# Kernel optimization log

Hardware: AMD Instinct MI355X
Metric: run time of the kernel (lower is better)

Reference implementation:

```python
import jax, jax.numpy as jnp
import numpy as np

B, C = 262144, 14  # batch, num_labels (CheXpert 14 labels)
MAX_T = C - 1      # max_num_trials
L_PARAM = 14       # self.l
KAPPA = 2.0
RAMP_CAP = 1.8     # 1 - s with s = -0.8


def setup_inputs() -> dict:
    key = jax.random.key(0)
    k1, k2, k3, k4 = jax.random.split(key, 4)
    inp = jax.random.normal(k1, (B, C), dtype=jnp.float32)
    target = jax.random.randint(k2, (B, C), 0, 2, dtype=jnp.int32)
    S = jax.random.uniform(k3, (B,), dtype=jnp.float32)
    # pre-drawn uniforms driving the sequential negative-sampling trials
    rand_u = jax.random.uniform(k4, (B, C, MAX_T), dtype=jnp.float32)
    return {"inp": inp, "target": target, "S": S, "rand_u": rand_u}


def reference(inp, target, S, rand_u):
    # L[i] = sum_{r=1..i+1} 1/r  (harmonic weights), indices 0..L_PARAM-1
    L = jnp.cumsum(1.0 / (jnp.arange(L_PARAM, dtype=inp.dtype) + 1.0))

    neg_mask = target == 0                      # [B,C]
    pos_mask = target == 1                      # [B,C]
    num_neg = neg_mask.sum(axis=1)              # [B]

    # negative label positions packed to the front of each row (stable)
    order = jnp.argsort(jnp.where(neg_mask, 0, 1), axis=1, stable=True)  # [B,C]

    rows = jnp.arange(B)[:, None, None]
    # uniform choice among the num_neg negatives, per (i, j, trial)
    t_idx = jnp.clip((rand_u * num_neg[:, None, None].astype(rand_u.dtype)).astype(jnp.int32),
                     0, jnp.maximum(num_neg - 1, 0)[:, None, None])       # [B,C,T]
    neg_sample = order[rows, t_idx]                                       # [B,C,T]

    # sequential trial loop: stop at first margin >= 0, cap at MAX_T trials
    margins = 1.0 - inp[:, :, None] + inp[rows, neg_sample]               # [B,C,T]
    nonneg = margins >= 0
    first = jnp.argmax(nonneg, axis=2)                                    # 0 if none
    num_trials = jnp.where(nonneg.any(axis=2), first + 1, MAX_T)          # [B,C]
    r_j = MAX_T // num_trials                                             # floor
    weight = L[r_j]                                                       # [B,C]

    # ramp(1 - inp[i,j] + inp[i,k]) = clip(inp[i,j] - inp[i,k], 0, 1.8)
    pairwise = jnp.clip(inp[:, :, None] - inp[:, None, :], 0.0, RAMP_CAP)  # [B,C(j),C(k)]
    neg_sum = jnp.sum(pairwise * neg_mask[:, None, :].astype(inp.dtype), axis=2)  # [B,C]

    # s_i = 1 for i <= l, else S[i - l]
    idx = jnp.arange(B)
    s_i = jnp.where(idx <= L_PARAM, 1.0, S[jnp.maximum(idx - L_PARAM, 0)])  # [B]

    valid = pos_mask & (num_neg > 0)[:, None]  # skip positives with no negatives
    loss_warp = jnp.sum(s_i[:, None] * jnp.where(valid, weight * neg_sum, 0.0))

    # kappa term: ramp(target * inp) over all labels
    ramp_k = jnp.clip(1.0 - target.astype(inp.dtype) * inp, 0.0, RAMP_CAP)
    loss_kappa = KAPPA * jnp.sum(s_i[:, None] * ramp_k)

    return loss_warp + loss_kappa
```

## Files before the change

### kernel.cpp

```cpp
#include <hip/hip_runtime.h>

#define CC   14
#define MAXT 13
#define TPB  256
#define RAMP_CAP 1.8f

__global__ __launch_bounds__(TPB) void rwl_kernel(
    const float* __restrict__ inp, const int* __restrict__ target,
    const float* __restrict__ S, const float* __restrict__ rand_u,
    float* __restrict__ out, int B)
{
    __shared__ float s_red[4];
    const int tid = threadIdx.x;
    const int row = blockIdx.x * TPB + tid;

    constexpr float H2  = 1.0f + 0.5f;
    constexpr float H3  = H2  + (1.0f/3.0f);
    constexpr float H4  = H3  + 0.25f;
    constexpr float H5  = H4  + 0.2f;
    constexpr float H6  = H5  + (1.0f/6.0f);
    constexpr float H7  = H6  + (1.0f/7.0f);
    constexpr float H8  = H7  + 0.125f;
    constexpr float H9  = H8  + (1.0f/9.0f);
    constexpr float H10 = H9  + 0.1f;
    constexpr float H11 = H10 + (1.0f/11.0f);
    constexpr float H12 = H11 + (1.0f/12.0f);
    constexpr float H13 = H12 + (1.0f/13.0f);
    constexpr float H14 = H13 + (1.0f/14.0f);

    float total = 0.f;
    if (row < B) {
        const float* xrow = inp + (size_t)row * CC;
        const int*   trow = target + (size_t)row * CC;

        float x[CC];
        #pragma unroll
        for (int k = 0; k < CC; ++k) x[k] = xrow[k];

        unsigned pm = 0; float kap = 0.f;
        #pragma unroll
        for (int k = 0; k < CC; ++k) {
            if (trow[k] != 0) {
                pm |= (1u << k);
                kap += fminf(fmaxf(1.0f - x[k], 0.f), RAMP_CAP);
            } else {
                kap += 1.0f;
            }
        }
        const int nn = CC - __popc(pm);

        float lw = 0.f;
        if (pm != 0u && nn > 0) {
            const float fnn = (float)nn;
            const float* pu = rand_u + (size_t)row * (CC * MAXT);
            #pragma unroll
            for (int j = 0; j < CC; ++j) {
                if ((pm >> j) & 1u) {
                    const float* uj = pu + j * MAXT;
                    float uv[8];
                    #pragma unroll
                    for (int t = 0; t < 8; ++t) uv[t] = uj[t];

                    const float m1 = 1.0f - x[j];
                    float nsum = 0.f; unsigned gm = 0; int cnt = 0;
                    #pragma unroll
                    for (int k = 0; k < CC; ++k) {
                        if (!((pm >> k) & 1u)) {
                            nsum += fminf(fmaxf(x[j] - x[k], 0.f), RAMP_CAP);
                            if (m1 + x[k] >= 0.f) gm |= (1u << cnt);
                            ++cnt;
                        }
                    }

                    unsigned bits = 0;
                    #pragma unroll
                    for (int t = 0; t < 8; ++t) {
                        int ti = (int)(uv[t] * fnn);
                        ti = ti < 0 ? 0 : ti;
                        ti = ti > nn - 1 ? nn - 1 : ti;
                        bits |= ((gm >> ti) & 1u) << t;
                    }
                    if (bits == 0u) {
                        #pragma unroll
                        for (int t = 8; t < MAXT; ++t) {
                            int ti = (int)(uj[t] * fnn);
                            ti = ti < 0 ? 0 : ti;
                            ti = ti > nn - 1 ? nn - 1 : ti;
                            bits |= ((gm >> ti) & 1u) << t;
                        }
                    }
                    const int nt = bits ? __ffs(bits) : MAXT;
                    const float wt = (nt == 1) ? H14 : (nt == 2) ? H7
                                   : (nt == 3) ? H5  : (nt == 4) ? H4
                                   : (nt <= 6) ? H3  : H2;
                    lw += wt * nsum;
                }
            }
        }
        const float si = (row <= 14) ? 1.0f : S[row - 14];
        total = si * (lw + 2.0f * kap);
    }

    #pragma unroll
    for (int off = 32; off > 0; off >>= 1)
        total += __shfl_down(total, off, 64);
    const int wave = tid >> 6;
    if ((tid & 63) == 0) s_red[wave] = total;
    __syncthreads();
    if (tid == 0)
        atomicAdd(out, s_red[0] + s_red[1] + s_red[2] + s_red[3]);
}

extern "C" void kernel_launch(void* const* d_in, const int* in_sizes, int n_in,
                              void* d_out, int out_size, void* d_ws, size_t ws_size,
                              hipStream_t stream) {
    const float* inp    = (const float*)d_in[0];
    const int*   target = (const int*)d_in[1];
    const float* S      = (const float*)d_in[2];
    const float* ru     = (const float*)d_in[3];
    float*       out    = (float*)d_out;
    const int B = in_sizes[2];

    hipMemsetAsync(out, 0, sizeof(float), stream);

    const int blocks = (B + TPB - 1) / TPB;
    rwl_kernel<<<blocks, TPB, 0, stream>>>(inp, target, S, ru, out, B);
}
```

Measured before the change: 55.56 us.

## Process two rows per thread with alignment-aware vectorized float4 loads

Each thread now handles a pair of rows, with templates on row parity so the 14-wide rows can be read using aligned float4/float2 loads of inputs and targets. The per-label random-uniform reads become three aligned float4 loads, using a compile-time shift that accounts for each label's offset within the 182-float row. The aim is fewer, wider memory transactions and more independent work per thread. In exchange it halves the thread count, roughly doubles register pressure, and over-fetches some unused uniforms.

```diff
diff --git a/kernel.cpp b/kernel.cpp
--- a/kernel.cpp
+++ b/kernel.cpp
@@ -5,101 +5,165 @@
 #define TPB  256
 #define RAMP_CAP 1.8f
 
+constexpr float H2  = 1.0f + 0.5f;
+constexpr float H3  = H2  + (1.0f/3.0f);
+constexpr float H4  = H3  + 0.25f;
+constexpr float H5  = H4  + 0.2f;
+constexpr float H6  = H5  + (1.0f/6.0f);
+constexpr float H7  = H6  + (1.0f/7.0f);
+constexpr float H14 = H7 + 0.125f + (1.0f/9.0f) + 0.1f + (1.0f/11.0f)
+                         + (1.0f/12.0f) + (1.0f/13.0f) + (1.0f/14.0f);
+
+template<int PAR, int J>
+__device__ __forceinline__ void do_label(unsigned pm, int nn, float fnn,
+                                         const float* __restrict__ rowF,
+                                         const float (&x)[CC], float& lw)
+{
+    if ((pm >> J) & 1u) {
+        constexpr int SH = (J + 2 * PAR) & 3;
+        const float* qp = rowF + (13 * J - SH);
+        float4 q0 = *(const float4*)(qp);
+        float4 q1 = *(const float4*)(qp + 4);
+        float4 q2 = *(const float4*)(qp + 8);
+        const float e[12] = {q0.x,q0.y,q0.z,q0.w, q1.x,q1.y,q1.z,q1.w,
+                             q2.x,q2.y,q2.z,q2.w};
+
+        const float m1 = 1.0f - x[J];
+        float nsum = 0.f; unsigned gm = 0; int cnt = 0;
+        #pragma unroll
+        for (int k = 0; k < CC; ++k) {
+            if (!((pm >> k) & 1u)) {
+                nsum += fminf(fmaxf(x[J] - x[k], 0.f), RAMP_CAP);
+                if (m1 + x[k] >= 0.f) gm |= (1u << cnt);
+                ++cnt;
+            }
+        }
+
+        unsigned bits = 0;
+        #pragma unroll
+        for (int t = 0; t < 8; ++t) {
+            int ti = (int)(e[SH + t] * fnn);
+            ti = ti < 0 ? 0 : ti;
+            ti = ti > nn - 1 ? nn - 1 : ti;
+            bits |= ((gm >> ti) & 1u) << t;
+        }
+        if (bits == 0u) {
+            #pragma unroll
+            for (int t = 8; t < MAXT; ++t) {
+                int ti = (int)(rowF[13 * J + t] * fnn);
+                ti = ti < 0 ? 0 : ti;
+                ti = ti > nn - 1 ? nn - 1 : ti;
+                bits |= ((gm >> ti) & 1u) << t;
+            }
+        }
+        const int nt = bits ? __ffs(bits) : MAXT;
+        const float wt = (nt == 1) ? H14 : (nt == 2) ? H7
+                       : (nt == 3) ? H5  : (nt == 4) ? H4
+                       : (nt <= 6) ? H3  : H2;
+        lw += wt * nsum;
+    }
+}
+
+template<int PAR>
+__device__ __forceinline__ float row_contrib(int row,
+    const float* __restrict__ inp, const int* __restrict__ target,
+    const float* __restrict__ S, const float* __restrict__ rand_u)
+{
+    float x[CC];
+    {
+        const float* b = inp + (size_t)row * CC;
+        if constexpr (PAR == 0) {
+            float4 a0 = *(const float4*)(b);
+            float4 a1 = *(const float4*)(b + 4);
+            float4 a2 = *(const float4*)(b + 8);
+            float2 a3 = *(const float2*)(b + 12);
+            x[0]=a0.x; x[1]=a0.y; x[2]=a0.z; x[3]=a0.w;
+            x[4]=a1.x; x[5]=a1.y; x[6]=a1.z; x[7]=a1.w;
+            x[8]=a2.x; x[9]=a2.y; x[10]=a2.z; x[11]=a2.w;
+            x[12]=a3.x; x[13]=a3.y;
+        } else {
+            float2 a0 = *(const float2*)(b);
+            float4 a1 = *(const float4*)(b + 2);
+            float4 a2 = *(const float4*)(b + 6);
+            float4 a3 = *(const float4*)(b + 10);
+            x[0]=a0.x; x[1]=a0.y;
+            x[2]=a1.x; x[3]=a1.y; x[4]=a1.z; x[5]=a1.w;
+            x[6]=a2.x; x[7]=a2.y; x[8]=a2.z; x[9]=a2.w;
+            x[10]=a3.x; x[11]=a3.y; x[12]=a3.z; x[13]=a3.w;
+        }
+    }
+    int tg[CC];
+    {
+        const int* b = target + (size_t)row * CC;
+        if constexpr (PAR == 0) {
+            int4 a0 = *(const int4*)(b);
+            int4 a1 = *(const int4*)(b + 4);
+            int4 a2 = *(const int4*)(b + 8);
+            int2 a3 = *(const int2*)(b + 12);
+            tg[0]=a0.x; tg[1]=a0.y; tg[2]=a0.z; tg[3]=a0.w;
+            tg[4]=a1.x; tg[5]=a1.y; tg[6]=a1.z; tg[7]=a1.w;
+            tg[8]=a2.x; tg[9]=a2.y; tg[10]=a2.z; tg[11]=a2.w;
+            tg[12]=a3.x; tg[13]=a3.y;
+        } else {
+            int2 a0 = *(const int2*)(b);
+            int4 a1 = *(const int4*)(b + 2);
+            int4 a2 = *(const int4*)(b + 6);
+            int4 a3 = *(const int4*)(b + 10);
+            tg[0]=a0.x; tg[1]=a0.y;
+            tg[2]=a1.x; tg[3]=a1.y; tg[4]=a1.z; tg[5]=a1.w;
+            tg[6]=a2.x; tg[7]=a2.y; tg[8]=a2.z; tg[9]=a2.w;
+            tg[10]=a3.x; tg[11]=a3.y; tg[12]=a3.z; tg[13]=a3.w;
+        }
+    }
+
+    unsigned pm = 0; float kap = 0.f;
+    #pragma unroll
+    for (int k = 0; k < CC; ++k) {
+        if (tg[k] != 0) {
+            pm |= (1u << k);
+            kap += fminf(fmaxf(1.0f - x[k], 0.f), RAMP_CAP);
+        } else {
+            kap += 1.0f;
+        }
+    }
+    const int nn = CC - __popc(pm);
+
+    float lw = 0.f;
+    if (pm != 0u && nn > 0) {
+        const float fnn = (float)nn;
+        const float* rowF = rand_u + (size_t)row * (CC * MAXT);
+        do_label<PAR, 0>(pm, nn, fnn, rowF, x, lw);
+        do_label<PAR, 1>(pm, nn, fnn, rowF, x, lw);
+        do_label<PAR, 2>(pm, nn, fnn, rowF, x, lw);
+        do_label<PAR, 3>(pm, nn, fnn, rowF, x, lw);
+        do_label<PAR, 4>(pm, nn, fnn, rowF, x, lw);
+        do_label<PAR, 5>(pm, nn, fnn, rowF, x, lw);
+        do_label<PAR, 6>(pm, nn, fnn, rowF, x, lw);
+        do_label<PAR, 7>(pm, nn, fnn, rowF, x, lw);
+        do_label<PAR, 8>(pm, nn, fnn, rowF, x, lw);
+        do_label<PAR, 9>(pm, nn, fnn, rowF, x, lw);
+        do_label<PAR,10>(pm, nn, fnn, rowF, x, lw);
+        do_label<PAR,11>(pm, nn, fnn, rowF, x, lw);
+        do_label<PAR,12>(pm, nn, fnn, rowF, x, lw);
+        do_label<PAR,13>(pm, nn, fnn, rowF, x, lw);
+    }
+    const float si = (row <= 14) ? 1.0f : S[row - 14];
+    return si * (lw + 2.0f * kap);
+}
+
 __global__ __launch_bounds__(TPB) void rwl_kernel(
     const float* __restrict__ inp, const int* __restrict__ target,
     const float* __restrict__ S, const float* __restrict__ rand_u,
     float* __restrict__ out, int B)
 {
     __shared__ float s_red[4];
-    const int tid = threadIdx.x;
-    const int row = blockIdx.x * TPB + tid;
-
-    constexpr float H2  = 1.0f + 0.5f;
-    constexpr float H3  = H2  + (1.0f/3.0f);
-    constexpr float H4  = H3  + 0.25f;
-    constexpr float H5  = H4  + 0.2f;
-    constexpr float H6  = H5  + (1.0f/6.0f);
-    constexpr float H7  = H6  + (1.0f/7.0f);
-    constexpr float H8  = H7  + 0.125f;
-    constexpr float H9  = H8  + (1.0f/9.0f);
-    constexpr float H10 = H9  + 0.1f;
-    constexpr float H11 = H10 + (1.0f/11.0f);
-    constexpr float H12 = H11 + (1.0f/12.0f);
-    constexpr float H13 = H12 + (1.0f/13.0f);
-    constexpr float H14 = H13 + (1.0f/14.0f);
+    const int tid  = threadIdx.x;
+    const int pair = blockIdx.x * TPB + tid;
+    const int r0 = pair * 2, r1 = r0 + 1;
 
     float total = 0.f;
-    if (row < B) {
-        const float* xrow = inp + (size_t)row * CC;
-        const int*   trow = target + (size_t)row * CC;
-
-        float x[CC];
-        #pragma unroll
-        for (int k = 0; k < CC; ++k) x[k] = xrow[k];
-
-        unsigned pm = 0; float kap = 0.f;
-        #pragma unroll
-        for (int k = 0; k < CC; ++k) {
-            if (trow[k] != 0) {
-                pm |= (1u << k);
-                kap += fminf(fmaxf(1.0f - x[k], 0.f), RAMP_CAP);
-            } else {
-                kap += 1.0f;
-            }
-        }
-        const int nn = CC - __popc(pm);
-
-        float lw = 0.f;
-        if (pm != 0u && nn > 0) {
-            const float fnn = (float)nn;
-            const float* pu = rand_u + (size_t)row * (CC * MAXT);
-            #pragma unroll
-            for (int j = 0; j < CC; ++j) {
-                if ((pm >> j) & 1u) {
-                    const float* uj = pu + j * MAXT;
-                    float uv[8];
-                    #pragma unroll
-                    for (int t = 0; t < 8; ++t) uv[t] = uj[t];
-
-                    const float m1 = 1.0f - x[j];
-                    float nsum = 0.f; unsigned gm = 0; int cnt = 0;
-                    #pragma unroll
-                    for (int k = 0; k < CC; ++k) {
-                        if (!((pm >> k) & 1u)) {
-                            nsum += fminf(fmaxf(x[j] - x[k], 0.f), RAMP_CAP);
-                            if (m1 + x[k] >= 0.f) gm |= (1u << cnt);
-                            ++cnt;
-                        }
-                    }
-
-                    unsigned bits = 0;
-                    #pragma unroll
-                    for (int t = 0; t < 8; ++t) {
-                        int ti = (int)(uv[t] * fnn);
-                        ti = ti < 0 ? 0 : ti;
-                        ti = ti > nn - 1 ? nn - 1 : ti;
-                        bits |= ((gm >> ti) & 1u) << t;
-                    }
-                    if (bits == 0u) {
-                        #pragma unroll
-                        for (int t = 8; t < MAXT; ++t) {
-                            int ti = (int)(uj[t] * fnn);
-                            ti = ti < 0 ? 0 : ti;
-                            ti = ti > nn - 1 ? nn - 1 : ti;
-                            bits |= ((gm >> ti) & 1u) << t;
-                        }
-                    }
-                    const int nt = bits ? __ffs(bits) : MAXT;
-                    const float wt = (nt == 1) ? H14 : (nt == 2) ? H7
-                                   : (nt == 3) ? H5  : (nt == 4) ? H4
-                                   : (nt <= 6) ? H3  : H2;
-                    lw += wt * nsum;
-                }
-            }
-        }
-        const float si = (row <= 14) ? 1.0f : S[row - 14];
-        total = si * (lw + 2.0f * kap);
-    }
+    if (r0 < B) total += row_contrib<0>(r0, inp, target, S, rand_u);
+    if (r1 < B) total += row_contrib<1>(r1, inp, target, S, rand_u);
 
     #pragma unroll
     for (int off = 32; off > 0; off >>= 1)
@@ -123,6 +187,7 @@
 
     hipMemsetAsync(out, 0, sizeof(float), stream);
 
-    const int blocks = (B + TPB - 1) / TPB;
+    const int pairs  = (B + 1) / 2;
+    const int blocks = (pairs + TPB - 1) / TPB;
     rwl_kernel<<<blocks, TPB, 0, stream>>>(inp, target, S, ru, out, B);
 }
```

New measurement: 51.13 us. 1.09x faster.

## Vectorize nontemporal loads and prefetch all trial uniforms branch-free

Applied to the files above, without the earlier changes.

Reads inp, target and the first eight trial uniforms of every label with 16-byte nontemporal vector loads, all issued up front. The per-label loop now runs branch-free, masking out non-positive labels instead of skipping them, and only loads trials 8-12 when needed. This is meant to cut load instruction count and divergence-induced latency serialization, at the cost of extra reads of uniforms for negative labels and higher register pressure. The tail loop also gains a gm!=0 early-out.

```diff
diff --git a/kernel.cpp b/kernel.cpp
--- a/kernel.cpp
+++ b/kernel.cpp
@@ -4,6 +4,20 @@
 #define MAXT 13
 #define TPB  256
 #define RAMP_CAP 1.8f
+
+constexpr float H2  = 1.0f + 0.5f;
+constexpr float H3  = H2  + (1.0f/3.0f);
+constexpr float H4  = H3  + 0.25f;
+constexpr float H5  = H4  + 0.2f;
+constexpr float H6  = H5  + (1.0f/6.0f);
+constexpr float H7  = H6  + (1.0f/7.0f);
+constexpr float H14 = H7 + 0.125f + (1.0f/9.0f) + 0.1f + (1.0f/11.0f)
+                         + (1.0f/12.0f) + (1.0f/13.0f) + (1.0f/14.0f);
+
+typedef float float4u __attribute__((ext_vector_type(4), aligned(4)));
+typedef float float2u __attribute__((ext_vector_type(2), aligned(4)));
+typedef int   int4u   __attribute__((ext_vector_type(4), aligned(4)));
+typedef int   int2u   __attribute__((ext_vector_type(2), aligned(4)));
 
 __global__ __launch_bounds__(TPB) void rwl_kernel(
     const float* __restrict__ inp, const int* __restrict__ target,
@@ -14,89 +28,87 @@
     const int tid = threadIdx.x;
     const int row = blockIdx.x * TPB + tid;
 
-    constexpr float H2  = 1.0f + 0.5f;
-    constexpr float H3  = H2  + (1.0f/3.0f);
-    constexpr float H4  = H3  + 0.25f;
-    constexpr float H5  = H4  + 0.2f;
-    constexpr float H6  = H5  + (1.0f/6.0f);
-    constexpr float H7  = H6  + (1.0f/7.0f);
-    constexpr float H8  = H7  + 0.125f;
-    constexpr float H9  = H8  + (1.0f/9.0f);
-    constexpr float H10 = H9  + 0.1f;
-    constexpr float H11 = H10 + (1.0f/11.0f);
-    constexpr float H12 = H11 + (1.0f/12.0f);
-    constexpr float H13 = H12 + (1.0f/13.0f);
-    constexpr float H14 = H13 + (1.0f/14.0f);
-
     float total = 0.f;
     if (row < B) {
-        const float* xrow = inp + (size_t)row * CC;
-        const int*   trow = target + (size_t)row * CC;
+        const float* xp = inp    + (size_t)row * CC;
+        const int*   tp = target + (size_t)row * CC;
+        const float* pu = rand_u + (size_t)row * (CC * MAXT);
 
-        float x[CC];
+        float4u xv0 = __builtin_nontemporal_load((const float4u*)(xp));
+        float4u xv1 = __builtin_nontemporal_load((const float4u*)(xp + 4));
+        float4u xv2 = __builtin_nontemporal_load((const float4u*)(xp + 8));
+        float2u xv3 = __builtin_nontemporal_load((const float2u*)(xp + 12));
+        int4u   tv0 = __builtin_nontemporal_load((const int4u*)(tp));
+        int4u   tv1 = __builtin_nontemporal_load((const int4u*)(tp + 4));
+        int4u   tv2 = __builtin_nontemporal_load((const int4u*)(tp + 8));
+        int2u   tv3 = __builtin_nontemporal_load((const int2u*)(tp + 12));
+
+        float4u q0[CC], q1[CC];
         #pragma unroll
-        for (int k = 0; k < CC; ++k) x[k] = xrow[k];
+        for (int j = 0; j < CC; ++j) {
+            q0[j] = __builtin_nontemporal_load((const float4u*)(pu + 13 * j));
+            q1[j] = __builtin_nontemporal_load((const float4u*)(pu + 13 * j + 4));
+        }
+
+        float x[CC] = {xv0.x,xv0.y,xv0.z,xv0.w, xv1.x,xv1.y,xv1.z,xv1.w,
+                       xv2.x,xv2.y,xv2.z,xv2.w, xv3.x,xv3.y};
+        const int tg[CC] = {tv0.x,tv0.y,tv0.z,tv0.w, tv1.x,tv1.y,tv1.z,tv1.w,
+                            tv2.x,tv2.y,tv2.z,tv2.w, tv3.x,tv3.y};
 
         unsigned pm = 0; float kap = 0.f;
         #pragma unroll
         for (int k = 0; k < CC; ++k) {
-            if (trow[k] != 0) {
+            if (tg[k] != 0) {
                 pm |= (1u << k);
                 kap += fminf(fmaxf(1.0f - x[k], 0.f), RAMP_CAP);
             } else {
                 kap += 1.0f;
             }
         }
-        const int nn = CC - __popc(pm);
+        const int   nn   = CC - __popc(pm);
+        const bool  vrow = (nn > 0);
+        const float fnn  = (float)nn;
 
         float lw = 0.f;
-        if (pm != 0u && nn > 0) {
-            const float fnn = (float)nn;
-            const float* pu = rand_u + (size_t)row * (CC * MAXT);
+        #pragma unroll
+        for (int j = 0; j < CC; ++j) {
+            const float e[8] = {q0[j].x,q0[j].y,q0[j].z,q0[j].w,
+                                q1[j].x,q1[j].y,q1[j].z,q1[j].w};
+            const float m1 = 1.0f - x[j];
+            float nsum = 0.f; unsigned gm = 0; int cnt = 0;
             #pragma unroll
-            for (int j = 0; j < CC; ++j) {
-                if ((pm >> j) & 1u) {
-                    const float* uj = pu + j * MAXT;
-                    float uv[8];
-                    #pragma unroll
-                    for (int t = 0; t < 8; ++t) uv[t] = uj[t];
-
-                    const float m1 = 1.0f - x[j];
-                    float nsum = 0.f; unsigned gm = 0; int cnt = 0;
-                    #pragma unroll
-                    for (int k = 0; k < CC; ++k) {
-                        if (!((pm >> k) & 1u)) {
-                            nsum += fminf(fmaxf(x[j] - x[k], 0.f), RAMP_CAP);
-                            if (m1 + x[k] >= 0.f) gm |= (1u << cnt);
-                            ++cnt;
-                        }
-                    }
-
-                    unsigned bits = 0;
-                    #pragma unroll
-                    for (int t = 0; t < 8; ++t) {
-                        int ti = (int)(uv[t] * fnn);
-                        ti = ti < 0 ? 0 : ti;
-                        ti = ti > nn - 1 ? nn - 1 : ti;
-                        bits |= ((gm >> ti) & 1u) << t;
-                    }
-                    if (bits == 0u) {
-                        #pragma unroll
-                        for (int t = 8; t < MAXT; ++t) {
-                            int ti = (int)(uj[t] * fnn);
-                            ti = ti < 0 ? 0 : ti;
-                            ti = ti > nn - 1 ? nn - 1 : ti;
-                            bits |= ((gm >> ti) & 1u) << t;
-                        }
-                    }
-                    const int nt = bits ? __ffs(bits) : MAXT;
-                    const float wt = (nt == 1) ? H14 : (nt == 2) ? H7
-                                   : (nt == 3) ? H5  : (nt == 4) ? H4
-                                   : (nt <= 6) ? H3  : H2;
-                    lw += wt * nsum;
+            for (int k = 0; k < CC; ++k) {
+                if (!((pm >> k) & 1u)) {
+                    nsum += fminf(fmaxf(x[j] - x[k], 0.f), RAMP_CAP);
+                    if (m1 + x[k] >= 0.f) gm |= (1u << cnt);
+                    ++cnt;
                 }
             }
+            unsigned bits = 0;
+            #pragma unroll
+            for (int t = 0; t < 8; ++t) {
+                int ti = (int)(e[t] * fnn);
+                ti = ti < 0 ? 0 : ti;
+                ti = ti > nn - 1 ? nn - 1 : ti;
+                bits |= ((gm >> ti) & 1u) << t;
+            }
+            const bool pos = (pm >> j) & 1u;
+            if (pos && vrow && bits == 0u && gm != 0u) {
+                #pragma unroll
+                for (int t = 8; t < MAXT; ++t) {
+                    int ti = (int)(pu[13 * j + t] * fnn);
+                    ti = ti < 0 ? 0 : ti;
+                    ti = ti > nn - 1 ? nn - 1 : ti;
+                    bits |= ((gm >> ti) & 1u) << t;
+                }
+            }
+            const int nt = bits ? __ffs(bits) : MAXT;
+            const float wt = (nt == 1) ? H14 : (nt == 2) ? H7
+                           : (nt == 3) ? H5  : (nt == 4) ? H4
+                           : (nt <= 6) ? H3  : H2;
+            lw += (pos && vrow) ? wt * nsum : 0.f;
         }
+
         const float si = (row <= 14) ? 1.0f : S[row - 14];
         total = si * (lw + 2.0f * kap);
     }
@@ -104,8 +116,7 @@
     #pragma unroll
     for (int off = 32; off > 0; off >>= 1)
         total += __shfl_down(total, off, 64);
-    const int wave = tid >> 6;
-    if ((tid & 63) == 0) s_red[wave] = total;
+    if ((tid & 63) == 0) s_red[tid >> 6] = total;
     __syncthreads();
     if (tid == 0)
         atomicAdd(out, s_red[0] + s_red[1] + s_red[2] + s_red[3]);
```

New measurement: 106.7 us. 1.92x slower.
